# Kernel tuning notes

Hardware: AMD Instinct MI355X
Metric: run time of the kernel (lower is better)

## Reference

```python
import jax, jax.numpy as jnp
import numpy as np
from jax import lax

NC = 80
REG_MAX = 16
BINS = REG_MAX + 1
RADIUS = 2.5
TOPK = 10
L_BOX, L_CLS, L_DFL = 7.5, 1.0, 1.5


def focal_bce(x, t, alpha=0.25, gamma=2.0):
    # numerically stable BCE-with-logits: max(x,0) - x*t + log1p(exp(-|x|))
    p = jax.nn.sigmoid(x)
    ce = jnp.maximum(x, 0.0) - x * t + jnp.log1p(jnp.exp(-jnp.abs(x)))
    p_t = p * t + (1.0 - p) * (1.0 - t)
    a_t = alpha * t + (1.0 - alpha) * (1.0 - t)
    return ce * a_t * (1.0 - p_t) ** gamma


def _level_loss(reg, cls, boxes, labels, stride):
    B, _, H, W = reg.shape
    HW = H * W
    G = boxes.shape[1]
    gy, gx = jnp.meshgrid(jnp.arange(H, dtype=jnp.float32), jnp.arange(W, dtype=jnp.float32), indexing='ij')
    centers = jnp.stack([gx + 0.5, gy + 0.5], -1).reshape(HW, 2)  # [HW,2]
    gt = boxes / stride  # [B,G,4]
    gctr = (gt[..., :2] + gt[..., 2:]) * 0.5  # [B,G,2]
    cx = centers[None, :, None, 0]
    cy = centers[None, :, None, 1]
    dl = cx - gt[:, None, :, 0]
    dt = cy - gt[:, None, :, 1]
    dr = gt[:, None, :, 2] - cx
    db = gt[:, None, :, 3] - cy
    in_gt = (dl > 0) & (dt > 0) & (dr > 0) & (db > 0)
    in_ctr = ((cx >= gctr[:, None, :, 0] - RADIUS) & (cx <= gctr[:, None, :, 0] + RADIUS)
              & (cy >= gctr[:, None, :, 1] - RADIUS) & (cy <= gctr[:, None, :, 1] + RADIUS))
    mask = in_gt & in_ctr  # [B,HW,G]
    any_pos = jnp.any(mask, axis=(1, 2))  # [B]
    # fallback: topk closest anchor centers per GT (smallest distance along point dim)
    dist = jnp.sqrt(((centers[None, :, None, :] - gctr[:, None, :, :]) ** 2).sum(-1))  # [B,HW,G]
    k = min(TOPK, HW)
    _, idx = lax.top_k(-jnp.swapaxes(dist, 1, 2), k)  # [B,G,k]
    fb = jnp.zeros((B, HW, G), bool).at[jnp.arange(B)[:, None, None], idx, jnp.arange(G)[None, :, None]].set(True)
    mask = jnp.where(any_pos[:, None, None], mask, fb)
    mf = mask.astype(jnp.float32)
    n_pos = mf.sum((1, 2))  # [B] (>=1 by construction of fallback)

    cls_flat = cls.transpose(0, 2, 3, 1).reshape(B, HW, NC)
    reg_flat = reg.transpose(0, 2, 3, 1).reshape(B, HW, 4, BINS)

    # ---- DFL ----
    ltrb = jnp.clip(jnp.stack([dl, dt, dr, db], -1), 0.0)  # [B,HW,G,4]
    tgt = jnp.clip(ltrb, 0.0, REG_MAX - 1e-4)
    lb = jnp.floor(tgt).astype(jnp.int32)
    rb = jnp.minimum(lb + 1, REG_MAX)
    wl = rb.astype(jnp.float32) - tgt
    wr = tgt - lb.astype(jnp.float32)
    logp = jax.nn.log_softmax(reg_flat, -1)  # [B,HW,4,BINS]
    bi = jnp.arange(B)[:, None, None, None]
    pi = jnp.arange(HW)[None, :, None, None]
    ki = jnp.arange(4)[None, None, None, :]
    dfl_pair = -(logp[bi, pi, ki, lb] * wl + logp[bi, pi, ki, rb] * wr)  # [B,HW,G,4]
    dfl = ((dfl_pair * mf[..., None]).sum((1, 2, 3)) / (n_pos * 4.0)).sum()

    # ---- box (IoU, detached as in original) ----
    prob = jax.nn.softmax(reg_flat, -1)
    d = (prob * jnp.arange(BINS, dtype=jnp.float32)).sum(-1)  # [B,HW,4]
    pcx = centers[None, :, 0]
    pcy = centers[None, :, 1]
    pred_box = jnp.stack([pcx - d[..., 0], pcy - d[..., 1], pcx + d[..., 2], pcy + d[..., 3]], -1)  # [B,HW,4]
    b1 = pred_box[:, :, None, :]
    b2 = gt[:, None, :, :]
    iw = jnp.clip(jnp.minimum(b1[..., 2:], b2[..., 2:]) - jnp.maximum(b1[..., :2], b2[..., :2]), 0.0)
    inter = iw[..., 0] * iw[..., 1]
    a1 = (b1[..., 2] - b1[..., 0]) * (b1[..., 3] - b1[..., 1])
    a2 = (b2[..., 2] - b2[..., 0]) * (b2[..., 3] - b2[..., 1])
    iou = lax.stop_gradient(inter / (a1 + a2 - inter + 1e-6))  # [B,HW,G]
    box = ((1.0 - iou) * mf).sum()

    # ---- cls (focal BCE, soft IoU targets). Decompose one-hot target:
    # per positive pair: sum_c f(logit_c,0) - f(logit_cls,0) + f(logit_cls,iou)
    fz = focal_bce(cls_flat, 0.0)  # [B,HW,NC]
    fz_sum = fz.sum(-1)  # [B,HW]
    bi2 = jnp.arange(B)[:, None, None]
    pi2 = jnp.arange(HW)[None, :, None]
    ci = labels[:, None, :]  # [B,1,G]
    cls_at = cls_flat[bi2, pi2, ci]  # [B,HW,G]
    fz_at = fz[bi2, pi2, ci]
    cls_pos = ((fz_sum[:, :, None] - fz_at + focal_bce(cls_at, iou)) * mf).sum()
    pos_pt = jnp.any(mask, -1)  # [B,HW]
    cls_neg = jnp.where(pos_pt, 0.0, fz_sum).sum()
    return box, cls_pos + cls_neg, dfl


def _total(reg0, cls0, reg1, cls1, reg2, cls2, gt_boxes, gt_labels):
    tb = tc = td = 0.0
    for r, c, s in ((reg0, cls0, 8.0), (reg1, cls1, 16.0), (reg2, cls2, 32.0)):
        b, cl, d = _level_loss(r, c, gt_boxes, gt_labels, s)
        tb = tb + b
        tc = tc + cl
        td = td + d
    loss = L_BOX * tb + L_CLS * tc + L_DFL * td
    return loss, tb, tc, td


def setup_inputs() -> dict:
    key = jax.random.key(0)
    ks = jax.random.split(key, 10)
    B, G = 16, 32
    d = {}
    for i, (h, w) in enumerate(((80, 80), (40, 40), (20, 20))):
        d[f'reg{i}'] = jax.random.normal(ks[2 * i], (B, 4 * BINS, h, w), jnp.float32)
        d[f'cls{i}'] = jax.random.normal(ks[2 * i + 1], (B, NC, h, w), jnp.float32)
    ctr = jax.random.uniform(ks[6], (B, G, 2), minval=0.0, maxval=640.0)
    wh = jax.random.uniform(ks[7], (B, G, 2), minval=16.0, maxval=160.0)
    x1y1 = jnp.clip(ctr - wh * 0.5, 0.0, 640.0)
    x2y2 = jnp.clip(ctr + wh * 0.5, 0.0, 640.0)
    d['gt_boxes'] = jnp.concatenate([x1y1, x2y2], -1)
    d['gt_labels'] = jax.random.randint(ks[8], (B, G), 0, NC, jnp.int32)
    return d


def reference(reg0, cls0, reg1, cls1, reg2, cls2, gt_boxes, gt_labels):
    return _total(reg0, cls0, reg1, cls1, reg2, cls2, gt_boxes, gt_labels)
```

## Files before the change

kernel.cpp:

```cpp
#include <hip/hip_runtime.h>
#include <math.h>

#define NCLS 80
#define BINS 17
#define REGMAX 16
#define NG 32
#define NB 16
#define KTOP 10
#define RAD 2.5f

#define WS_ACC   0
#define WS_NPOS  32
#define WS_DFLN  224
#define WS_ANYP  416
#define WS_CNT   608
#define WS_FB    640
#define NBLOCKS  (67 * 16)

__device__ __forceinline__ float focal0(float x) {
    float e   = __expf(-fabsf(x));
    float inv = 1.0f / (1.0f + e);
    float p   = (x >= 0.0f) ? inv : e * inv;
    float ce  = fmaxf(x, 0.0f) + __logf(1.0f + e);
    return ce * 0.75f * p * p;
}

__device__ __forceinline__ float focal_t(float x, float t) {
    float e   = __expf(-fabsf(x));
    float inv = 1.0f / (1.0f + e);
    float p   = (x >= 0.0f) ? inv : e * inv;
    float ce  = fmaxf(x, 0.0f) - x * t + __logf(1.0f + e);
    float pt  = p * t + (1.0f - p) * (1.0f - t);
    float at  = 0.25f * t + 0.75f * (1.0f - t);
    float om  = 1.0f - pt;
    return ce * at * om * om;
}

__global__ void k_prep(const float* __restrict__ gtb,
                       float* __restrict__ acc, float* __restrict__ npos,
                       float* __restrict__ dfln, int* __restrict__ anyp,
                       int* __restrict__ cnt, int* __restrict__ fb) {
    int lvl = blockIdx.x;
    int tid = threadIdx.x;
    int b = tid >> 5, g = tid & 31;
    int W = (lvl == 0) ? 80 : (lvl == 1 ? 40 : 20);
    float inv_s = (lvl == 0) ? 0.125f : (lvl == 1 ? 0.0625f : 0.03125f);
    if (lvl == 0) {
        if (tid < 2)  acc[tid] = 0.0f;
        if (tid < 48) { npos[tid] = 0.0f; dfln[tid] = 0.0f; }
        if (tid == 48) *cnt = 0;
    }
    __shared__ int s_any[NB];
    if (tid < NB) s_any[tid] = 0;
    __syncthreads();

    const float* bb = gtb + (b * NG + g) * 4;
    float x1 = bb[0] * inv_s, y1 = bb[1] * inv_s;
    float x2 = bb[2] * inv_s, y2 = bb[3] * inv_s;
    float gcx = (x1 + x2) * 0.5f, gcy = (y1 + y2) * 0.5f;
    int j0 = max((int)floorf(gcx) - 4, 0), j1 = min((int)floorf(gcx) + 4, W - 1);
    int i0 = max((int)floorf(gcy) - 4, 0), i1 = min((int)floorf(gcy) + 4, W - 1);
    bool any = false;
    for (int i = i0; i <= i1; ++i) {
        float cy = (float)i + 0.5f;
        for (int j = j0; j <= j1; ++j) {
            float cx = (float)j + 0.5f;
            bool m = (cx - x1 > 0.0f) && (cy - y1 > 0.0f) &&
                     (x2 - cx > 0.0f) && (y2 - cy > 0.0f) &&
                     (cx >= gcx - RAD) && (cx <= gcx + RAD) &&
                     (cy >= gcy - RAD) && (cy <= gcy + RAD);
            any = any || m;
        }
    }
    if (any) atomicOr(&s_any[b], 1);
    __syncthreads();
    if (g == 0) anyp[lvl * NB + b] = s_any[b];

    if (!s_any[b]) {
        float bd[KTOP]; int bi[KTOP];
        for (int t = 0; t < KTOP; ++t) { bd[t] = 3.0e38f; bi[t] = 0; }
        int HW = W * W;
        for (int p = 0; p < HW; ++p) {
            float cx = (float)(p % W) + 0.5f;
            float cy = (float)(p / W) + 0.5f;
            float dx = cx - gcx, dy = cy - gcy;
            float d = dx * dx + dy * dy;
            if (d < bd[KTOP - 1]) {
                int t = KTOP - 1;
                while (t > 0 && d < bd[t - 1]) { bd[t] = bd[t-1]; bi[t] = bi[t-1]; --t; }
                bd[t] = d; bi[t] = p;
            }
        }
        int* o = fb + ((lvl * NB + b) * NG + g) * KTOP;
        for (int t = 0; t < KTOP; ++t) o[t] = bi[t];
    }
}

__global__ __launch_bounds__(256) void k_main_f(
    const float* __restrict__ reg0, const float* __restrict__ cls0,
    const float* __restrict__ reg1, const float* __restrict__ cls1,
    const float* __restrict__ reg2, const float* __restrict__ cls2,
    const float* __restrict__ gtb,  const int* __restrict__ lab,
    const int* __restrict__ anyp,   const int* __restrict__ fb,
    float* __restrict__ acc, float* __restrict__ npos, float* __restrict__ dfln,
    int* __restrict__ cnt, float* __restrict__ out)
{
    int bx = blockIdx.x;
    int b  = blockIdx.y;
    int lvl, tix, W; const float *regp, *clsp; float inv_s;
    if (bx < 50)      { lvl = 0; tix = bx;      W = 80; regp = reg0; clsp = cls0; inv_s = 0.125f;   }
    else if (bx < 63) { lvl = 1; tix = bx - 50; W = 40; regp = reg1; clsp = cls1; inv_s = 0.0625f;  }
    else              { lvl = 2; tix = bx - 63; W = 20; regp = reg2; clsp = cls2; inv_s = 0.03125f; }
    int HW = W * W;
    int tile = tix * 128;

    int lane = threadIdx.x & 63;
    int s    = threadIdx.x >> 6;
    int q0   = tile + 2 * lane;
    bool v   = q0 < HW;
    int qc   = v ? q0 : 0;
    int ri0  = qc / W, ci0 = qc - ri0 * W;
    float cx0 = (float)ci0 + 0.5f, cy0 = (float)ri0 + 0.5f;
    int ci1 = ci0 + 1, ri1 = ri0; if (ci1 == W) { ci1 = 0; ri1 = ri0 + 1; }
    float cx1 = (float)ci1 + 0.5f, cy1 = (float)ri1 + 0.5f;

    int base_r = (b * 4 * BINS) * HW + qc;
    int base_c = (b * NCLS) * HW + qc;

    __shared__ float s_dv[4][128], s_lz[4][128], s_fz[4][128];
    __shared__ unsigned char s_ps[4][128];

    {
        float2 xv[BINS];
#pragma unroll
        for (int t = 0; t < BINS; ++t)
            xv[t] = v ? *(const float2*)(regp + base_r + (s * BINS + t) * HW)
                      : make_float2(0.0f, 0.0f);
        float m0 = xv[0].x, m1 = xv[0].y;
#pragma unroll
        for (int t = 1; t < BINS; ++t) { m0 = fmaxf(m0, xv[t].x); m1 = fmaxf(m1, xv[t].y); }
        float sa = 0.f, ea = 0.f, sb = 0.f, eb = 0.f;
#pragma unroll
        for (int t = 0; t < BINS; ++t) {
            float a = __expf(xv[t].x - m0), c = __expf(xv[t].y - m1);
            sa += a; ea += a * (float)t; sb += c; eb += c * (float)t;
        }
        s_dv[s][2*lane]   = ea / sa;  s_lz[s][2*lane]   = __logf(sa) + m0;
        s_dv[s][2*lane+1] = eb / sb;  s_lz[s][2*lane+1] = __logf(sb) + m1;
    }
    {
        float fz0 = 0.f, fz1 = 0.f;
#pragma unroll 4
        for (int t = 0; t < 20; ++t) {
            float2 c2 = v ? *(const float2*)(clsp + base_c + (s * 20 + t) * HW)
                          : make_float2(0.0f, 0.0f);
            fz0 += focal0(c2.x); fz1 += focal0(c2.y);
        }
        s_fz[s][2*lane] = fz0; s_fz[s][2*lane+1] = fz1;
    }
    __syncthreads();

    float dv0[4], lz0v[4], dv1[4], lz1v[4];
#pragma unroll
    for (int k = 0; k < 4; ++k) {
        dv0[k] = s_dv[k][2*lane];   lz0v[k] = s_lz[k][2*lane];
        dv1[k] = s_dv[k][2*lane+1]; lz1v[k] = s_lz[k][2*lane+1];
    }
    float fzs0 = s_fz[0][2*lane]   + s_fz[1][2*lane]   + s_fz[2][2*lane]   + s_fz[3][2*lane];
    float fzs1 = s_fz[0][2*lane+1] + s_fz[1][2*lane+1] + s_fz[2][2*lane+1] + s_fz[3][2*lane+1];

    float px1_0 = cx0 - dv0[0], py1_0 = cy0 - dv0[1];
    float px2_0 = cx0 + dv0[2], py2_0 = cy0 + dv0[3];
    float pa0 = (px2_0 - px1_0) * (py2_0 - py1_0);
    float px1_1 = cx1 - dv1[0], py1_1 = cy1 - dv1[1];
    float px2_1 = cx1 + dv1[2], py2_1 = cy1 + dv1[3];
    float pa1 = (px2_1 - px1_1) * (py2_1 - py1_1);

    bool anyb = anyp[lvl * NB + b] != 0;
    float bxa = 0.f, cla = 0.f, dfa = 0.f, np = 0.f;
    bool posi0 = false, posi1 = false;

#define HEAVY(G, CX, CY, DL, DT, DR, DB, PX1, PY1, PX2, PY2, PA, LZ, FZS, OFF) do { \
    float ix1 = fmaxf(PX1, x1), iy1 = fmaxf(PY1, y1);                    \
    float ix2 = fminf(PX2, x2), iy2 = fminf(PY2, y2);                    \
    float iw = fmaxf(ix2 - ix1, 0.f), ih = fmaxf(iy2 - iy1, 0.f);        \
    float inter = iw * ih;                                               \
    float ga = (x2 - x1) * (y2 - y1);                                    \
    float iou = inter / (PA + ga - inter + 1e-6f);                       \
    bxa += 1.f - iou; np += 1.f;                                         \
    float ltrb[4] = { DL, DT, DR, DB };                                  \
    _Pragma("unroll")                                                    \
    for (int k = 0; k < 4; ++k) {                                        \
        float tt = fminf(fmaxf(ltrb[k], 0.f), 15.9999f);                 \
        float lf = floorf(tt); int lb = (int)lf;                         \
        int rb = lb + 1 > REGMAX ? REGMAX : lb + 1;                      \
        float wl = (float)rb - tt, wr = tt - lf;                         \
        float xl = regp[base_r + OFF + (k * BINS + lb) * HW];            \
        float xr = regp[base_r + OFF + (k * BINS + rb) * HW];            \
        dfa -= (xl - LZ[k]) * wl + (xr - LZ[k]) * wr;                    \
    }                                                                    \
    int c = lab[b * NG + G];                                             \
    float xat = clsp[base_c + OFF + c * HW];                             \
    cla += FZS - focal0(xat) + focal_t(xat, iou);                        \
} while (0)

#define PROC_G(G, GEOM) do {                                             \
    const float* bbp = gtb + (b * NG + (G)) * 4;                         \
    float x1 = bbp[0] * inv_s, y1 = bbp[1] * inv_s;                      \
    float x2 = bbp[2] * inv_s, y2 = bbp[3] * inv_s;                      \
    float dl0 = cx0 - x1, dt0 = cy0 - y1, dr0 = x2 - cx0, db0 = y2 - cy0;\
    float dl1 = cx1 - x1, dt1 = cy1 - y1, dr1 = x2 - cx1, db1 = y2 - cy1;\
    bool m0, m1;                                                         \
    if (GEOM) {                                                          \
        float gx = (x1 + x2) * 0.5f, gy = (y1 + y2) * 0.5f;              \
        m0 = (dl0 > 0.f) && (dt0 > 0.f) && (dr0 > 0.f) && (db0 > 0.f) && \
             (cx0 >= gx - RAD) && (cx0 <= gx + RAD) &&                   \
             (cy0 >= gy - RAD) && (cy0 <= gy + RAD);                     \
        m1 = (dl1 > 0.f) && (dt1 > 0.f) && (dr1 > 0.f) && (db1 > 0.f) && \
             (cx1 >= gx - RAD) && (cx1 <= gx + RAD) &&                   \
             (cy1 >= gy - RAD) && (cy1 <= gy + RAD);                     \
    } else {                                                             \
        const int* fbp = fb + ((lvl * NB + b) * NG + (G)) * KTOP;        \
        m0 = false; m1 = false;                                          \
        _Pragma("unroll")                                                \
        for (int t = 0; t < KTOP; ++t) {                                 \
            int f = fbp[t]; m0 = m0 || (f == q0); m1 = m1 || (f == q0+1);\
        }                                                                \
    }                                                                    \
    m0 = m0 && v; m1 = m1 && v;                                          \
    if (__any(m0 || m1)) {                                               \
        if (m0) HEAVY((G), cx0, cy0, dl0, dt0, dr0, db0,                 \
                      px1_0, py1_0, px2_0, py2_0, pa0, lz0v, fzs0, 0);   \
        if (m1) HEAVY((G), cx1, cy1, dl1, dt1, dr1, db1,                 \
                      px1_1, py1_1, px2_1, py2_1, pa1, lz1v, fzs1, 1);   \
    }                                                                    \
    posi0 = posi0 || m0; posi1 = posi1 || m1;                            \
} while (0)

    if (anyb) {
        int gg = lane & 31;
        const float* bbg = gtb + (b * NG + gg) * 4;
        float gy1 = bbg[1] * inv_s, gy2 = bbg[3] * inv_s;
        float gcy = (gy1 + gy2) * 0.5f;
        int r0 = tile / W;
        int r1 = min(tile + 127, HW - 1) / W;
        float cyLo = (float)r0 + 0.5f, cyHi = (float)r1 + 0.5f;
        bool act = (cyHi > gy1) && (gy2 > cyLo) &&
                   (cyHi >= gcy - RAD) && (cyLo <= gcy + RAD);
        unsigned long long bm = __ballot(act);
        unsigned m32 = (unsigned)(bm | (bm >> 32));
        int ord = 0;
        while (m32) {
            int g = __builtin_ctz(m32); m32 &= m32 - 1;
            if ((ord++ & 3) == s) PROC_G(g, true);
        }
    } else {
        for (int t = 0; t < 8; ++t) { int g = s * 8 + t; PROC_G(g, false); }
    }

    s_ps[s][2*lane] = posi0; s_ps[s][2*lane+1] = posi1;
    __syncthreads();
    if (s == 0) {
        int pg0 = s_ps[0][2*lane] | s_ps[1][2*lane] | s_ps[2][2*lane] | s_ps[3][2*lane];
        int pg1 = s_ps[0][2*lane+1] | s_ps[1][2*lane+1] | s_ps[2][2*lane+1] | s_ps[3][2*lane+1];
        if (v && !pg0) cla += fzs0;
        if (v && !pg1) cla += fzs1;
    }

    float v0 = bxa, v1 = cla, v2 = dfa, v3 = np;
    for (int off = 32; off > 0; off >>= 1) {
        v0 += __shfl_down(v0, off);
        v1 += __shfl_down(v1, off);
        v2 += __shfl_down(v2, off);
        v3 += __shfl_down(v3, off);
    }
    __shared__ float red[4][4];
    if (lane == 0) { red[s][0] = v0; red[s][1] = v1; red[s][2] = v2; red[s][3] = v3; }
    __syncthreads();
    if (threadIdx.x == 0) {
        float t0 = 0, t1 = 0, t2 = 0, t3 = 0;
        for (int w = 0; w < 4; ++w) {
            t0 += red[w][0]; t1 += red[w][1]; t2 += red[w][2]; t3 += red[w][3];
        }
        atomicAdd(&acc[0], t0);
        atomicAdd(&acc[1], t1);
        atomicAdd(&dfln[lvl * NB + b], t2);
        atomicAdd(&npos[lvl * NB + b], t3);
    }

    __shared__ int s_tick;
    if (threadIdx.x == 0) {
        __threadfence();
        s_tick = atomicAdd(cnt, 1);
    }
    __syncthreads();
    if (s_tick == NBLOCKS - 1 && threadIdx.x < 64) {
        float vs = 0.f;
        if (lane < 48) {
            float n = atomicAdd(&npos[lane], 0.0f);
            float d = atomicAdd(&dfln[lane], 0.0f);
            if (n > 0.f) vs = d / (n * 4.0f);
        }
        for (int off = 32; off > 0; off >>= 1) vs += __shfl_down(vs, off);
        if (lane == 0) {
            float tbv = atomicAdd(&acc[0], 0.0f);
            float tcv = atomicAdd(&acc[1], 0.0f);
            out[0] = 7.5f * tbv + tcv + 1.5f * vs;
            out[1] = tbv; out[2] = tcv; out[3] = vs;
        }
    }
}

extern "C" void kernel_launch(void* const* d_in, const int* in_sizes, int n_in,
                              void* d_out, int out_size, void* d_ws, size_t ws_size,
                              hipStream_t stream) {
    const float* reg0 = (const float*)d_in[0];
    const float* cls0 = (const float*)d_in[1];
    const float* reg1 = (const float*)d_in[2];
    const float* cls1 = (const float*)d_in[3];
    const float* reg2 = (const float*)d_in[4];
    const float* cls2 = (const float*)d_in[5];
    const float* gtb  = (const float*)d_in[6];
    const int*   lab  = (const int*)d_in[7];
    float* out = (float*)d_out;

    char*  ws   = (char*)d_ws;
    float* acc  = (float*)(ws + WS_ACC);
    float* npos = (float*)(ws + WS_NPOS);
    float* dfln = (float*)(ws + WS_DFLN);
    int*   anyp = (int*)(ws + WS_ANYP);
    int*   cnt  = (int*)(ws + WS_CNT);
    int*   fb   = (int*)(ws + WS_FB);

    k_prep<<<3, 512, 0, stream>>>(gtb, acc, npos, dfln, anyp, cnt, fb);
    k_main_f<<<dim3(67, NB), 256, 0, stream>>>(reg0, cls0, reg1, cls1, reg2, cls2,
                                               gtb, lab, anyp, fb,
                                               acc, npos, dfln, cnt, out);
}
```

Before: 68.70 us.

## Hoist all reg/cls loads upfront, stage GT boxes and labels in LDS

Issues all 17 reg and 20 cls float2 loads before any compute so more memory requests are in flight at once. It also stages the scaled GT boxes, their centres and labels in shared memory so the per-GT loop stops re-reading global memory. The launch bounds now request 4 blocks per CU. Dropping the validity guard on the loads relies on qc being clamped to 0 for invalid lanes, and holding 37 float2 values live raises register pressure, which may conflict with the occupancy target.

```diff
diff --git a/kernel.cpp b/kernel.cpp
--- a/kernel.cpp
+++ b/kernel.cpp
@@ -96,7 +96,7 @@
     }
 }
 
-__global__ __launch_bounds__(256) void k_main_f(
+__global__ __launch_bounds__(256, 4) void k_main_f(
     const float* __restrict__ reg0, const float* __restrict__ cls0,
     const float* __restrict__ reg1, const float* __restrict__ cls1,
     const float* __restrict__ reg2, const float* __restrict__ cls2,
@@ -129,20 +129,36 @@
 
     __shared__ float s_dv[4][128], s_lz[4][128], s_fz[4][128];
     __shared__ unsigned char s_ps[4][128];
+    __shared__ float s_bx[NG][6];
+    __shared__ int   s_lab[NG];
+
+    if (threadIdx.x < NG) {
+        int g = threadIdx.x;
+        float4 bb4 = *(const float4*)(gtb + (b * NG + g) * 4);
+        float x1 = bb4.x * inv_s, y1 = bb4.y * inv_s;
+        float x2 = bb4.z * inv_s, y2 = bb4.w * inv_s;
+        s_bx[g][0] = x1; s_bx[g][1] = y1; s_bx[g][2] = x2; s_bx[g][3] = y2;
+        s_bx[g][4] = (x1 + x2) * 0.5f; s_bx[g][5] = (y1 + y2) * 0.5f;
+        s_lab[g] = lab[b * NG + g];
+    }
+
+    float2 rv[BINS];
+#pragma unroll
+    for (int t = 0; t < BINS; ++t)
+        rv[t] = *(const float2*)(regp + base_r + (s * BINS + t) * HW);
+    float2 cv[20];
+#pragma unroll
+    for (int t = 0; t < 20; ++t)
+        cv[t] = *(const float2*)(clsp + base_c + (s * 20 + t) * HW);
 
     {
-        float2 xv[BINS];
-#pragma unroll
-        for (int t = 0; t < BINS; ++t)
-            xv[t] = v ? *(const float2*)(regp + base_r + (s * BINS + t) * HW)
-                      : make_float2(0.0f, 0.0f);
-        float m0 = xv[0].x, m1 = xv[0].y;
-#pragma unroll
-        for (int t = 1; t < BINS; ++t) { m0 = fmaxf(m0, xv[t].x); m1 = fmaxf(m1, xv[t].y); }
+        float m0 = rv[0].x, m1 = rv[0].y;
+#pragma unroll
+        for (int t = 1; t < BINS; ++t) { m0 = fmaxf(m0, rv[t].x); m1 = fmaxf(m1, rv[t].y); }
         float sa = 0.f, ea = 0.f, sb = 0.f, eb = 0.f;
 #pragma unroll
         for (int t = 0; t < BINS; ++t) {
-            float a = __expf(xv[t].x - m0), c = __expf(xv[t].y - m1);
+            float a = __expf(rv[t].x - m0), c = __expf(rv[t].y - m1);
             sa += a; ea += a * (float)t; sb += c; eb += c * (float)t;
         }
         s_dv[s][2*lane]   = ea / sa;  s_lz[s][2*lane]   = __logf(sa) + m0;
@@ -150,12 +166,8 @@
     }
     {
         float fz0 = 0.f, fz1 = 0.f;
-#pragma unroll 4
-        for (int t = 0; t < 20; ++t) {
-            float2 c2 = v ? *(const float2*)(clsp + base_c + (s * 20 + t) * HW)
-                          : make_float2(0.0f, 0.0f);
-            fz0 += focal0(c2.x); fz1 += focal0(c2.y);
-        }
+#pragma unroll
+        for (int t = 0; t < 20; ++t) { fz0 += focal0(cv[t].x); fz1 += focal0(cv[t].y); }
         s_fz[s][2*lane] = fz0; s_fz[s][2*lane+1] = fz1;
     }
     __syncthreads();
@@ -199,20 +211,19 @@
         float xr = regp[base_r + OFF + (k * BINS + rb) * HW];            \
         dfa -= (xl - LZ[k]) * wl + (xr - LZ[k]) * wr;                    \
     }                                                                    \
-    int c = lab[b * NG + G];                                             \
+    int c = s_lab[G];                                                    \
     float xat = clsp[base_c + OFF + c * HW];                             \
     cla += FZS - focal0(xat) + focal_t(xat, iou);                        \
 } while (0)
 
 #define PROC_G(G, GEOM) do {                                             \
-    const float* bbp = gtb + (b * NG + (G)) * 4;                         \
-    float x1 = bbp[0] * inv_s, y1 = bbp[1] * inv_s;                      \
-    float x2 = bbp[2] * inv_s, y2 = bbp[3] * inv_s;                      \
+    float x1 = s_bx[G][0], y1 = s_bx[G][1];                              \
+    float x2 = s_bx[G][2], y2 = s_bx[G][3];                              \
     float dl0 = cx0 - x1, dt0 = cy0 - y1, dr0 = x2 - cx0, db0 = y2 - cy0;\
     float dl1 = cx1 - x1, dt1 = cy1 - y1, dr1 = x2 - cx1, db1 = y2 - cy1;\
     bool m0, m1;                                                         \
     if (GEOM) {                                                          \
-        float gx = (x1 + x2) * 0.5f, gy = (y1 + y2) * 0.5f;              \
+        float gx = s_bx[G][4], gy = s_bx[G][5];                          \
         m0 = (dl0 > 0.f) && (dt0 > 0.f) && (dr0 > 0.f) && (db0 > 0.f) && \
              (cx0 >= gx - RAD) && (cx0 <= gx + RAD) &&                   \
              (cy0 >= gy - RAD) && (cy0 <= gy + RAD);                     \
@@ -239,9 +250,7 @@
 
     if (anyb) {
         int gg = lane & 31;
-        const float* bbg = gtb + (b * NG + gg) * 4;
-        float gy1 = bbg[1] * inv_s, gy2 = bbg[3] * inv_s;
-        float gcy = (gy1 + gy2) * 0.5f;
+        float gy1 = s_bx[gg][1], gy2 = s_bx[gg][3], gcy = s_bx[gg][5];
         int r0 = tile / W;
         int r1 = min(tile + 127, HW - 1) / W;
         float cyLo = (float)r0 + 0.5f, cyHi = (float)r1 + 0.5f;
```

Result: no change. 69.30 us (+0.9%).
